# Optimization experiments

Measured on AMD Instinct MI355X. Metric: run time of the kernel, lower is better.

The kernel has to match this reference:

```python
import math
from itertools import permutations
import jax, jax.numpy as jnp
import numpy as np

L, M, D, F, E, N = 64, 3, 3, 32, 8, 100000
PERMS = np.array(list(permutations(range(M))), dtype=np.int32)  # [P, M], P = M! = 6
HALF_PI = math.pi / 2.0
EPS = 1e-8  # torch CosineSimilarity eps


def _atan_inv(s):
    return jnp.arctan(1.0 / s)


def _intra_angle(p):
    # cosine similarity between each row and the previous row (roll by 1 on support axis)
    q = jnp.roll(p, 1, axis=-2)
    num = jnp.sum(q * p, axis=-1)
    den = jnp.maximum(jnp.linalg.norm(q, axis=-1) * jnp.linalg.norm(p, axis=-1), EPS)
    return num / den


def setup_inputs() -> dict:
    key = jax.random.key(0)
    ks = jax.random.split(key, 9)
    return {
        "x_focal": jax.random.normal(ks[0], (N, F), jnp.float32),
        "p_focal": jax.random.normal(ks[1], (N, D), jnp.float32),
        "x_neighbor": jax.random.normal(ks[2], (N, M, F), jnp.float32),
        "p_neighbor": jax.random.normal(ks[3], (N, M, D), jnp.float32),
        "edge_attr_neighbor": jax.random.normal(ks[4], (N, M, E), jnp.float32),
        "x_center": jax.random.normal(ks[5], (L, 1, F), jnp.float32),
        "x_support": jax.random.normal(ks[6], (L, M, F), jnp.float32),
        "edge_attr_support": jax.random.normal(ks[7], (L, M, E), jnp.float32),
        "p_support": jax.random.normal(ks[8], (L, M, D), jnp.float32),
    }


def reference(x_focal, p_focal, x_neighbor, p_neighbor, edge_attr_neighbor,
              x_center, x_support, edge_attr_support, p_support):
    perms = jnp.asarray(PERMS)

    # --- support attribute score over all permutations: sum_{m,f}(x_nei - xs_perm)^2 ---
    xs_p = x_support[:, perms]                                   # [L,P,M,F]
    nei_sq = jnp.sum(x_neighbor * x_neighbor, axis=(1, 2))       # [N]
    sup_sq = jnp.sum(xs_p * xs_p, axis=(2, 3))                   # [L,P]
    cross = jnp.einsum('nmf,lpmf->lpn', x_neighbor, xs_p)        # [L,P,N]
    support_all = _atan_inv(nei_sq[None, None, :] + sup_sq[..., None] - 2.0 * cross)
    best_idx = jnp.argmax(support_all, axis=1)                   # [L,N]
    support_sc = jnp.max(support_all, axis=1)                    # [L,N]

    def select_best(all_sc):  # [L,P,N] -> [L,N] at best permutation
        return jnp.take_along_axis(all_sc, best_idx[:, None, :], axis=1)[:, 0]

    # relative neighbor positions
    p_rel = p_neighbor - p_focal[:, None, :]                     # [N,M,D]
    ps_p = p_support[:, perms]                                   # [L,P,M,D]

    # --- angle score: intra-row cosine angles, then arctan(1/sum_m diff^2) ---
    ang_nei = _intra_angle(p_rel)                                # [N,M]
    ang_sup = _intra_angle(ps_p)                                 # [L,P,M]
    dang = (jnp.sum(ang_nei * ang_nei, axis=-1)[None, None, :]
            + jnp.sum(ang_sup * ang_sup, axis=-1)[..., None]
            - 2.0 * jnp.einsum('nm,lpm->lpn', ang_nei, ang_sup))
    angle_sc = select_best(_atan_inv(dang))                      # [L,N]

    # --- length score: row norms ---
    len_nei = jnp.linalg.norm(p_rel, axis=-1)                    # [N,M]
    len_sup = jnp.linalg.norm(ps_p, axis=-1)                     # [L,P,M]
    dlen = (jnp.sum(len_nei * len_nei, axis=-1)[None, None, :]
            + jnp.sum(len_sup * len_sup, axis=-1)[..., None]
            - 2.0 * jnp.einsum('nm,lpm->lpn', len_nei, len_sup))
    length_sc = select_best(_atan_inv(dlen))                     # [L,N]

    # --- center attribute score ---
    xc = x_center[:, 0, :]                                       # [L,F]
    dc = (jnp.sum(x_focal * x_focal, axis=-1)[None, :]
          + jnp.sum(xc * xc, axis=-1)[:, None]
          - 2.0 * jnp.einsum('nf,lf->ln', x_focal, xc))
    center_sc = _atan_inv(dc)                                    # [L,N]

    # --- edge attribute score ---
    es_p = edge_attr_support[:, perms]                           # [L,P,M,E]
    dedge = (jnp.sum(edge_attr_neighbor ** 2, axis=(1, 2))[None, None, :]
             + jnp.sum(es_p * es_p, axis=(2, 3))[..., None]
             - 2.0 * jnp.einsum('nme,lpme->lpn', edge_attr_neighbor, es_p))
    edge_sc = select_best(_atan_inv(dedge))                      # [L,N]

    # --- total score ---
    h = ((length_sc - HALF_PI) ** 2 + (angle_sc - HALF_PI) ** 2
         + (support_sc - HALF_PI) ** 2 + (center_sc - HALF_PI) ** 2
         + (edge_sc - HALF_PI) ** 2)
    return jnp.arctan(1.0 / h)                                   # [L,N]
```

## Files before the change

### kernel.cpp

```cpp
#include <hip/hip_runtime.h>
#include <math.h>

#define L_ 64
#define HPf 1.57079632679489661923f
#define TIE_THR 4e-3f

typedef _Float16 half4 __attribute__((ext_vector_type(4)));
typedef float    f32x4 __attribute__((ext_vector_type(4)));

#define CVT4(H, L, V) {                                                       \
    _Float16 h0=(_Float16)(V).x, h1=(_Float16)(V).y,                          \
             h2=(_Float16)(V).z, h3=(_Float16)(V).w;                          \
    (H) = (half4){h0, h1, h2, h3};                                            \
    (L) = (half4){(_Float16)((V).x-(float)h0), (_Float16)((V).y-(float)h1),   \
                  (_Float16)((V).z-(float)h2), (_Float16)((V).w-(float)h3)};  \
}

#define MFMA6T(ACC, T, M)                                                           \
    ACC = __builtin_amdgcn_mfma_f32_16x16x16f16(sh[T][0], nh[M][0], ACC, 0, 0, 0); \
    ACC = __builtin_amdgcn_mfma_f32_16x16x16f16(sh[T][0], nl[M][0], ACC, 0, 0, 0); \
    ACC = __builtin_amdgcn_mfma_f32_16x16x16f16(sl[T][0], nh[M][0], ACC, 0, 0, 0); \
    ACC = __builtin_amdgcn_mfma_f32_16x16x16f16(sh[T][1], nh[M][1], ACC, 0, 0, 0); \
    ACC = __builtin_amdgcn_mfma_f32_16x16x16f16(sh[T][1], nl[M][1], ACC, 0, 0, 0); \
    ACC = __builtin_amdgcn_mfma_f32_16x16x16f16(sl[T][1], nh[M][1], ACC, 0, 0, 0);

#define MFMA3(ACC, AH, AL, BH, BL)                                           \
    ACC = __builtin_amdgcn_mfma_f32_16x16x16f16((AH), (BH), ACC, 0, 0, 0);   \
    ACC = __builtin_amdgcn_mfma_f32_16x16x16f16((AH), (BL), ACC, 0, 0, 0);   \
    ACC = __builtin_amdgcn_mfma_f32_16x16x16f16((AL), (BH), ACC, 0, 0, 0);

__global__ __launch_bounds__(64)
void setconvP(const float* __restrict__ x_support,
              const float* __restrict__ edge_sup,
              const float* __restrict__ x_center,
              const float* __restrict__ p_support,
              float* __restrict__ table)
{
    const int l = threadIdx.x;
    if (l >= L_) return;

    const float* xs = x_support + (size_t)l * 96;
    double ssq = 0.0;
    for (int i = 0; i < 96; ++i) { double v = (double)xs[i]; ssq += v * v; }

    const float* es = edge_sup + (size_t)l * 24;
    float esq = 0.f;
    for (int i = 0; i < 24; ++i) esq = fmaf(es[i], es[i], esq);

    const float* xc = x_center + (size_t)l * 32;
    float csq = 0.f;
    for (int i = 0; i < 32; ++i) csq = fmaf(xc[i], xc[i], csq);

    float p0[3], p1[3], p2[3];
    for (int d = 0; d < 3; ++d) {
        p0[d] = p_support[(l * 3 + 0) * 3 + d];
        p1[d] = p_support[(l * 3 + 1) * 3 + d];
        p2[d] = p_support[(l * 3 + 2) * 3 + d];
    }
    float n0 = sqrtf(p0[0]*p0[0] + p0[1]*p0[1] + p0[2]*p0[2]);
    float n1 = sqrtf(p1[0]*p1[0] + p1[1]*p1[1] + p1[2]*p1[2]);
    float n2 = sqrtf(p2[0]*p2[0] + p2[1]*p2[1] + p2[2]*p2[2]);
    float d01 = p0[0]*p1[0] + p0[1]*p1[1] + p0[2]*p1[2];
    float d02 = p0[0]*p2[0] + p0[1]*p2[1] + p0[2]*p2[2];
    float d12 = p1[0]*p2[0] + p1[1]*p2[1] + p1[2]*p2[2];
    float C01 = d01 / fmaxf(n0 * n1, 1e-8f);
    float C02 = d02 / fmaxf(n0 * n2, 1e-8f);
    float C12 = d12 / fmaxf(n1 * n2, 1e-8f);

    float* t = table + l * 16;
    t[0] = n0;  t[1] = n1;  t[2] = n2;
    t[3] = C01; t[4] = C02; t[5] = C12;
    t[6] = C01*C01 + C02*C02 + C12*C12;
    t[7] = n0*n0 + n1*n1 + n2*n2;
    t[8] = esq;
    t[9] = csq;
    t[10] = (float)ssq;
}

__global__ __launch_bounds__(64)
void setconvF(const float* __restrict__ x_neighbor,
              const float* __restrict__ x_support,
              const float* __restrict__ x_focal,
              const float* __restrict__ p_focal,
              const float* __restrict__ p_neighbor,
              const float* __restrict__ edge_nei,
              const float* __restrict__ x_center,
              const float* __restrict__ edge_sup,
              const float* __restrict__ table,
              float* __restrict__ out,
              int* __restrict__ wl_cnt,
              int* __restrict__ wl,
              int wl_cap, int N)
{
    const int lane = threadIdx.x;
    const int j    = lane & 15;
    const int kg   = lane >> 4;
    const int l_w  = blockIdx.y * 16;
    const int n_start = blockIdx.x * 64;

    const float4 z4 = make_float4(0.f, 0.f, 0.f, 0.f);

    half4 sh[4][2], sl[4][2];
    half4 esh[4], esl[4];
    half4 xch[2], xcl[2];
    {
        const int g = j >> 2, e = j & 3;
        #pragma unroll
        for (int t = 0; t < 4; ++t) {
            float4 v0 = z4, v1 = z4, ve = z4;
            if (e < 3) {
                const float* ap = x_support + (size_t)(l_w + 4*t + g) * 96 + e * 32 + kg * 4;
                v0 = *(const float4*)ap;
                v1 = *(const float4*)(ap + 16);
                if (kg < 2)
                    ve = *(const float4*)(edge_sup + (size_t)(l_w + 4*t + g) * 24 + e * 8 + kg * 4);
            }
            CVT4(sh[t][0], sl[t][0], v0);
            CVT4(sh[t][1], sl[t][1], v1);
            CVT4(esh[t], esl[t], ve);
        }
        const int l_c = l_w + 4 * (j & 3) + (j >> 2);
        #pragma unroll
        for (int h = 0; h < 2; ++h) {
            float4 v = *(const float4*)(x_center + (size_t)l_c * 32 + 16*h + kg * 4);
            CVT4(xch[h], xcl[h], v);
        }
    }

    #pragma unroll 1
    for (int c = 0; c < 4; ++c) {
        const int n_j = n_start + c * 16 + j;
        const bool ok = (n_j < N);

        float4 w0h0=z4,w0h1=z4,w1h0=z4,w1h1=z4,w2h0=z4,w2h1=z4;
        float4 ef0=z4, ef1=z4, ef2=z4;
        float4 xf0=z4, xf1=z4;
        float pf0=0.f,pf1=0.f,pf2=0.f;
        float pn0=0.f,pn1=0.f,pn2=0.f,pn3=0.f,pn4=0.f,pn5=0.f,pn6=0.f,pn7=0.f,pn8=0.f;
        if (ok) {
            const float* np = x_neighbor + (size_t)n_j * 96 + kg * 4;
            w0h0 = *(const float4*)(np +  0); w0h1 = *(const float4*)(np + 16);
            w1h0 = *(const float4*)(np + 32); w1h1 = *(const float4*)(np + 48);
            w2h0 = *(const float4*)(np + 64); w2h1 = *(const float4*)(np + 80);
            if (kg < 2) {
                const float* ep = edge_nei + (size_t)n_j * 24 + kg * 4;
                ef0 = *(const float4*)(ep +  0);
                ef1 = *(const float4*)(ep +  8);
                ef2 = *(const float4*)(ep + 16);
            }
            const float* fp = x_focal + (size_t)n_j * 32 + kg * 4;
            xf0 = *(const float4*)(fp + 0);
            xf1 = *(const float4*)(fp + 16);
            pf0 = p_focal[(size_t)n_j*3+0]; pf1 = p_focal[(size_t)n_j*3+1]; pf2 = p_focal[(size_t)n_j*3+2];
            const float* pp = p_neighbor + (size_t)n_j * 9;
            pn0=pp[0]; pn1=pp[1]; pn2=pp[2]; pn3=pp[3]; pn4=pp[4];
            pn5=pp[5]; pn6=pp[6]; pn7=pp[7]; pn8=pp[8];
        }

        float rp = 0.f;
        rp = fmaf(w0h0.x, w0h0.x, rp); rp = fmaf(w0h0.y, w0h0.y, rp);
        rp = fmaf(w0h0.z, w0h0.z, rp); rp = fmaf(w0h0.w, w0h0.w, rp);
        rp = fmaf(w0h1.x, w0h1.x, rp); rp = fmaf(w0h1.y, w0h1.y, rp);
        rp = fmaf(w0h1.z, w0h1.z, rp); rp = fmaf(w0h1.w, w0h1.w, rp);
        rp = fmaf(w1h0.x, w1h0.x, rp); rp = fmaf(w1h0.y, w1h0.y, rp);
        rp = fmaf(w1h0.z, w1h0.z, rp); rp = fmaf(w1h0.w, w1h0.w, rp);
        rp = fmaf(w1h1.x, w1h1.x, rp); rp = fmaf(w1h1.y, w1h1.y, rp);
        rp = fmaf(w1h1.z, w1h1.z, rp); rp = fmaf(w1h1.w, w1h1.w, rp);
        rp = fmaf(w2h0.x, w2h0.x, rp); rp = fmaf(w2h0.y, w2h0.y, rp);
        rp = fmaf(w2h0.z, w2h0.z, rp); rp = fmaf(w2h0.w, w2h0.w, rp);
        rp = fmaf(w2h1.x, w2h1.x, rp); rp = fmaf(w2h1.y, w2h1.y, rp);
        rp = fmaf(w2h1.z, w2h1.z, rp); rp = fmaf(w2h1.w, w2h1.w, rp);
        rp += __shfl_xor(rp, 16);
        rp += __shfl_xor(rp, 32);

        float edsq = 0.f;
        edsq = fmaf(ef0.x, ef0.x, edsq); edsq = fmaf(ef0.y, ef0.y, edsq);
        edsq = fmaf(ef0.z, ef0.z, edsq); edsq = fmaf(ef0.w, ef0.w, edsq);
        edsq = fmaf(ef1.x, ef1.x, edsq); edsq = fmaf(ef1.y, ef1.y, edsq);
        edsq = fmaf(ef1.z, ef1.z, edsq); edsq = fmaf(ef1.w, ef1.w, edsq);
        edsq = fmaf(ef2.x, ef2.x, edsq); edsq = fmaf(ef2.y, ef2.y, edsq);
        edsq = fmaf(ef2.z, ef2.z, edsq); edsq = fmaf(ef2.w, ef2.w, edsq);
        edsq += __shfl_xor(edsq, 16);
        edsq += __shfl_xor(edsq, 32);

        float xfsq = 0.f;
        xfsq = fmaf(xf0.x, xf0.x, xfsq); xfsq = fmaf(xf0.y, xf0.y, xfsq);
        xfsq = fmaf(xf0.z, xf0.z, xfsq); xfsq = fmaf(xf0.w, xf0.w, xfsq);
        xfsq = fmaf(xf1.x, xf1.x, xfsq); xfsq = fmaf(xf1.y, xf1.y, xfsq);
        xfsq = fmaf(xf1.z, xf1.z, xfsq); xfsq = fmaf(xf1.w, xf1.w, xfsq);
        xfsq += __shfl_xor(xfsq, 16);
        xfsq += __shfl_xor(xfsq, 32);

        float pr00=pn0-pf0, pr01=pn1-pf1, pr02=pn2-pf2;
        float pr10=pn3-pf0, pr11=pn4-pf1, pr12=pn5-pf2;
        float pr20=pn6-pf0, pr21=pn7-pf1, pr22=pn8-pf2;
        float lenN0 = sqrtf(pr00*pr00 + pr01*pr01 + pr02*pr02);
        float lenN1 = sqrtf(pr10*pr10 + pr11*pr11 + pr12*pr12);
        float lenN2 = sqrtf(pr20*pr20 + pr21*pr21 + pr22*pr22);
        float angN0 = (pr20*pr00 + pr21*pr01 + pr22*pr02) / fmaxf(lenN2*lenN0, 1e-8f);
        float angN1 = (pr00*pr10 + pr01*pr11 + pr02*pr12) / fmaxf(lenN0*lenN1, 1e-8f);
        float angN2 = (pr10*pr20 + pr11*pr21 + pr12*pr22) / fmaxf(lenN1*lenN2, 1e-8f);
        float angN_sq = angN0*angN0 + angN1*angN1 + angN2*angN2;
        float lenN_sq = lenN0*lenN0 + lenN1*lenN1 + lenN2*lenN2;

        half4 nh[3][2], nl[3][2];
        CVT4(nh[0][0], nl[0][0], w0h0); CVT4(nh[0][1], nl[0][1], w0h1);
        CVT4(nh[1][0], nl[1][0], w1h0); CVT4(nh[1][1], nl[1][1], w1h1);
        CVT4(nh[2][0], nl[2][0], w2h0); CVT4(nh[2][1], nl[2][1], w2h1);
        half4 edh0, edl0, edh1, edl1, edh2, edl2;
        CVT4(edh0, edl0, ef0); CVT4(edh1, edl1, ef1); CVT4(edh2, edl2, ef2);
        half4 xfh0, xfl0, xfh1, xfl1;
        CVT4(xfh0, xfl0, xf0); CVT4(xfh1, xfl1, xf1);

        f32x4 accC = {};
        MFMA3(accC, xch[0], xcl[0], xfh0, xfl0)
        MFMA3(accC, xch[1], xcl[1], xfh1, xfl1)

        #pragma unroll
        for (int t = 0; t < 4; ++t) {
            const int l_t = l_w + 4*t + kg;
            const float* tb = table + l_t * 16;
            f32x4 tb0 = *(const f32x4*)tb;
            f32x4 tb1 = *(const f32x4*)(tb + 4);
            f32x4 tb2 = *(const f32x4*)(tb + 8);

            f32x4 a0 = {}, a1 = {}, a2 = {};
            MFMA6T(a0, t, 0)
            MFMA6T(a1, t, 1)
            MFMA6T(a2, t, 2)

            f32x4 e0 = {}, e1 = {}, e2 = {};
            MFMA3(e0, esh[t], esl[t], edh0, edl0)
            MFMA3(e1, esh[t], esl[t], edh1, edl1)
            MFMA3(e2, esh[t], esl[t], edh2, edl2)

            float c0 = a0[0] + a1[1] + a2[2];
            float c1 = a0[0] + a1[2] + a2[1];
            float c2 = a0[1] + a1[0] + a2[2];
            float c3 = a0[1] + a1[2] + a2[0];
            float c4 = a0[2] + a1[0] + a2[1];
            float c5 = a0[2] + a1[1] + a2[0];

            float b1 = c0, b2 = -3.4e38f; int bpk = 6;
            if (c1 > b1) { b2 = b1; b1 = c1; bpk = 9;  } else if (c1 > b2) b2 = c1;
            if (c2 > b1) { b2 = b1; b1 = c2; bpk = 18; } else if (c2 > b2) b2 = c2;
            if (c3 > b1) { b2 = b1; b1 = c3; bpk = 24; } else if (c3 > b2) b2 = c3;
            if (c4 > b1) { b2 = b1; b1 = c4; bpk = 33; } else if (c4 > b2) b2 = c4;
            if (c5 > b1) { b2 = b1; b1 = c5; bpk = 36; } else if (c5 > b2) b2 = c5;

            const int a = (bpk >> 4) & 3, b = (bpk >> 2) & 3, cc = bpk & 3;

            float se0 = (a  == 0) ? e0[0] : ((a  == 1) ? e0[1] : e0[2]);
            float se1 = (b  == 0) ? e1[0] : ((b  == 1) ? e1[1] : e1[2]);
            float se2 = (cc == 0) ? e2[0] : ((cc == 1) ? e2[1] : e2[2]);
            float bestE = se0 + se1 + se2;

            float la = (a  == 0) ? tb0[0] : ((a  == 1) ? tb0[1] : tb0[2]);
            float lb = (b  == 0) ? tb0[0] : ((b  == 1) ? tb0[1] : tb0[2]);
            float lc = (cc == 0) ? tb0[0] : ((cc == 1) ? tb0[1] : tb0[2]);
            float bestL = fmaf(lenN0, la, fmaf(lenN1, lb, lenN2 * lc));

            float C01 = tb0[3], C02 = tb1[0], C12 = tb1[1];
            int sca = cc + a, sab = a + b, sbc = b + cc;
            float Cca = (sca == 1) ? C01 : ((sca == 2) ? C02 : C12);
            float Cab = (sab == 1) ? C01 : ((sab == 2) ? C02 : C12);
            float Cbc = (sbc == 1) ? C01 : ((sbc == 2) ? C02 : C12);
            float bestA = fmaf(angN0, Cca, fmaf(angN1, Cab, angN2 * Cbc));

            float dist = rp + tb2[2] - 2.0f * b1;
            float t3v = atanf(dist);
            float t1v = atanf(lenN_sq + tb1[3] - 2.0f * bestL);
            float t2v = atanf(angN_sq + tb1[2] - 2.0f * bestA);
            float t4v = atanf(xfsq    + tb2[1] - 2.0f * accC[t]);
            float t5v = atanf(edsq    + tb2[0] - 2.0f * bestE);

            float h = t1v*t1v + t2v*t2v + t3v*t3v + t4v*t4v + t5v*t5v;

            if (ok) {
                size_t idx = (size_t)l_t * N + n_j;
                out[idx] = atanf(1.0f / h);
                if (b1 - b2 <= TIE_THR) {
                    int slot = atomicAdd(wl_cnt, 1);
                    if (slot < wl_cap) wl[slot] = (int)idx;
                }
            }
        }
    }
}

__global__ __launch_bounds__(256)
void setconvA2(const float* __restrict__ x_neighbor,
               const float* __restrict__ x_support,
               const float* __restrict__ x_focal,
               const float* __restrict__ p_focal,
               const float* __restrict__ p_neighbor,
               const float* __restrict__ edge_nei,
               const float* __restrict__ x_center,
               const float* __restrict__ edge_sup,
               const float* __restrict__ table,
               float* __restrict__ out,
               const int* __restrict__ wl_cnt,
               const int* __restrict__ wl,
               int wl_cap, int N)
{
    int cnt = *wl_cnt; if (cnt > wl_cap) cnt = wl_cap;
    const int stride = gridDim.x * blockDim.x;
    for (int i = blockIdx.x * blockDim.x + threadIdx.x; i < cnt; i += stride) {
        const int idx = wl[i];
        const int l = idx / N;
        const int n = idx - l * N;
        const float* xn = x_neighbor + (size_t)n * 96;
        const float* xs = x_support  + (size_t)l * 96;

        double dr[3][3] = {{0,0,0},{0,0,0},{0,0,0}};
        double nei = 0.0;
        for (int f = 0; f < 32; ++f) {
            double a0 = (double)xn[f], a1 = (double)xn[32 + f], a2 = (double)xn[64 + f];
            double b0 = (double)xs[f], b1 = (double)xs[32 + f], b2 = (double)xs[64 + f];
            dr[0][0] += a0 * b0; dr[0][1] += a0 * b1; dr[0][2] += a0 * b2;
            dr[1][0] += a1 * b0; dr[1][1] += a1 * b1; dr[1][2] += a1 * b2;
            dr[2][0] += a2 * b0; dr[2][1] += a2 * b1; dr[2][2] += a2 * b2;
            nei += a0 * a0 + a1 * a1 + a2 * a2;
        }
        double d0 = dr[0][0] + dr[1][1] + dr[2][2];
        double d1 = dr[0][0] + dr[1][2] + dr[2][1];
        double d2 = dr[0][1] + dr[1][0] + dr[2][2];
        double d3 = dr[0][1] + dr[1][2] + dr[2][0];
        double d4 = dr[0][2] + dr[1][0] + dr[2][1];
        double d5 = dr[0][2] + dr[1][1] + dr[2][0];
        double db = d0; int bpk = 6;
        if (d1 > db) { db = d1; bpk = 9;  }
        if (d2 > db) { db = d2; bpk = 18; }
        if (d3 > db) { db = d3; bpk = 24; }
        if (d4 > db) { db = d4; bpk = 33; }
        if (d5 > db) { db = d5; bpk = 36; }
        const int a = (bpk >> 4) & 3, b = (bpk >> 2) & 3, c = bpk & 3;

        const float* tb = table + l * 16;
        float dist = (float)(nei + (double)tb[10] - 2.0 * db);
        float t3v = atanf(dist);

        const float* es = edge_sup + (size_t)l * 24;
        const float* ed = edge_nei + (size_t)n * 24;
        float er[3][3] = {{0,0,0},{0,0,0},{0,0,0}};
        for (int f = 0; f < 8; ++f) {
            float b0 = es[f], b1 = es[8 + f], b2 = es[16 + f];
            float a0 = ed[f], a1 = ed[8 + f], a2 = ed[16 + f];
            er[0][0] = fmaf(a0, b0, er[0][0]);
            er[0][1] = fmaf(a0, b1, er[0][1]);
            er[0][2] = fmaf(a0, b2, er[0][2]);
            er[1][0] = fmaf(a1, b0, er[1][0]);
            er[1][1] = fmaf(a1, b1, er[1][1]);
            er[1][2] = fmaf(a1, b2, er[1][2]);
            er[2][0] = fmaf(a2, b0, er[2][0]);
            er[2][1] = fmaf(a2, b1, er[2][1]);
            er[2][2] = fmaf(a2, b2, er[2][2]);
        }
        float edsq = 0.f;
        for (int f = 0; f < 24; ++f) edsq = fmaf(ed[f], ed[f], edsq);

        const float* xf = x_focal + (size_t)n * 32;
        const float* xc = x_center + (size_t)l * 32;
        float cdot = 0.f, xfsq = 0.f;
        for (int f = 0; f < 32; ++f) {
            cdot = fmaf(xf[f], xc[f], cdot);
            xfsq = fmaf(xf[f], xf[f], xfsq);
        }

        float pf0 = p_focal[(size_t)n*3+0], pf1 = p_focal[(size_t)n*3+1], pf2 = p_focal[(size_t)n*3+2];
        const float* pp = p_neighbor + (size_t)n * 9;
        float pr00=pp[0]-pf0, pr01=pp[1]-pf1, pr02=pp[2]-pf2;
        float pr10=pp[3]-pf0, pr11=pp[4]-pf1, pr12=pp[5]-pf2;
        float pr20=pp[6]-pf0, pr21=pp[7]-pf1, pr22=pp[8]-pf2;
        float lenN0 = sqrtf(pr00*pr00 + pr01*pr01 + pr02*pr02);
        float lenN1 = sqrtf(pr10*pr10 + pr11*pr11 + pr12*pr12);
        float lenN2 = sqrtf(pr20*pr20 + pr21*pr21 + pr22*pr22);
        float angN0 = (pr20*pr00 + pr21*pr01 + pr22*pr02) / fmaxf(lenN2*lenN0, 1e-8f);
        float angN1 = (pr00*pr10 + pr01*pr11 + pr02*pr12) / fmaxf(lenN0*lenN1, 1e-8f);
        float angN2 = (pr10*pr20 + pr11*pr21 + pr12*pr22) / fmaxf(lenN1*lenN2, 1e-8f);
        float angN_sq = angN0*angN0 + angN1*angN1 + angN2*angN2;
        float lenN_sq = lenN0*lenN0 + lenN1*lenN1 + lenN2*lenN2;

        float bestE = er[0][a] + er[1][b] + er[2][c];
        float nv[3] = {tb[0], tb[1], tb[2]};
        float bestL = fmaf(lenN0, nv[a], fmaf(lenN1, nv[b], lenN2 * nv[c]));
        float C01 = tb[3], C02 = tb[4], C12 = tb[5];
        int sca = c + a, sab = a + b, sbc = b + c;
        float Cca = (sca == 1) ? C01 : ((sca == 2) ? C02 : C12);
        float Cab = (sab == 1) ? C01 : ((sab == 2) ? C02 : C12);
        float Cbc = (sbc == 1) ? C01 : ((sbc == 2) ? C02 : C12);
        float bestA = fmaf(angN0, Cca, fmaf(angN1, Cab, angN2 * Cbc));

        float t1v = atanf(lenN_sq + tb[7] - 2.0f * bestL);
        float t2v = atanf(angN_sq + tb[6] - 2.0f * bestA);
        float t4v = atanf(xfsq    + tb[9] - 2.0f * cdot);
        float t5v = atanf(edsq    + tb[8] - 2.0f * bestE);

        float h = t1v*t1v + t2v*t2v + t3v*t3v + t4v*t4v + t5v*t5v;
        out[idx] = atanf(1.0f / h);
    }
}

extern "C" void kernel_launch(void* const* d_in, const int* in_sizes, int n_in,
                              void* d_out, int out_size, void* d_ws, size_t ws_size,
                              hipStream_t stream)
{
    const float* x_focal    = (const float*)d_in[0];
    const float* p_focal    = (const float*)d_in[1];
    const float* x_neighbor = (const float*)d_in[2];
    const float* p_neighbor = (const float*)d_in[3];
    const float* edge_nei   = (const float*)d_in[4];
    const float* x_center   = (const float*)d_in[5];
    const float* x_support  = (const float*)d_in[6];
    const float* edge_sup   = (const float*)d_in[7];
    const float* p_support  = (const float*)d_in[8];
    float* out = (float*)d_out;

    const int N = in_sizes[0] / 32;

    float* table = (float*)d_ws;
    int* wl_cnt = (int*)((char*)d_ws + 4096);
    int* wl     = (int*)((char*)d_ws + 4096 + 16);
    long cap_l = ((long)ws_size - 4096 - 16) / 4;
    int wl_cap = cap_l < 0 ? 0 : (cap_l > 4000000 ? 4000000 : (int)cap_l);

    hipMemsetAsync(wl_cnt, 0, sizeof(int), stream);

    setconvP<<<1, 64, 0, stream>>>(x_support, edge_sup, x_center, p_support, table);

    dim3 gridF((N + 63) / 64, 4);
    setconvF<<<gridF, 64, 0, stream>>>(x_neighbor, x_support, x_focal, p_focal,
                                       p_neighbor, edge_nei, x_center, edge_sup,
                                       table, out, wl_cnt, wl, wl_cap, N);
    setconvA2<<<64, 256, 0, stream>>>(x_neighbor, x_support, x_focal, p_focal,
                                      p_neighbor, edge_nei, x_center, edge_sup,
                                      table, out, wl_cnt, wl, wl_cap, N);
}
```

Baseline: 134.8 us.

## Precompute per-neighbor geometry, prefetch next chunk, and use polynomial atan

Adds a small kernel that computes per-neighbor lengths and angle cosines once and stores eight floats per neighbor, instead of recomputing them in each of the four L-block launches of the main kernel. The main kernel now loads the next 16-neighbor chunk ahead of computing the current one, to hide global memory latency. It also replaces atanf calls with a degree-9 polynomial plus hardware reciprocal. Costs are an extra launch, a workspace layout change, and reduced atan accuracy that may interact with the tie-handling threshold.

```diff
diff --git a/kernel.cpp b/kernel.cpp
--- a/kernel.cpp
+++ b/kernel.cpp
@@ -28,6 +28,28 @@
     ACC = __builtin_amdgcn_mfma_f32_16x16x16f16((AH), (BH), ACC, 0, 0, 0);   \
     ACC = __builtin_amdgcn_mfma_f32_16x16x16f16((AH), (BL), ACC, 0, 0, 0);   \
     ACC = __builtin_amdgcn_mfma_f32_16x16x16f16((AL), (BH), ACC, 0, 0, 0);
+
+__device__ __forceinline__ float atan_poly01(float t) {
+    float t2 = t * t;
+    float p = fmaf(t2, 0.0208351f, -0.0851330f);
+    p = fmaf(t2, p, 0.1801410f);
+    p = fmaf(t2, p, -0.3302995f);
+    p = fmaf(t2, p, 0.9998660f);
+    return t * p;
+}
+__device__ __forceinline__ float fast_atan_abs(float x) {
+    float ax = fabsf(x);
+    float r  = __builtin_amdgcn_rcpf(ax);
+    bool inv = ax > 1.0f;
+    float p  = atan_poly01(inv ? r : ax);
+    return inv ? (HPf - p) : p;
+}
+__device__ __forceinline__ float fast_atan_recip(float h) {
+    float r  = __builtin_amdgcn_rcpf(h);
+    bool inv = h > 1.0f;
+    float p  = atan_poly01(inv ? r : h);
+    return inv ? p : (HPf - p);
+}
 
 __global__ __launch_bounds__(64)
 void setconvP(const float* __restrict__ x_support,
@@ -77,16 +99,41 @@
     t[10] = (float)ssq;
 }
 
+__global__ __launch_bounds__(256)
+void setconvPn(const float* __restrict__ p_focal,
+               const float* __restrict__ p_neighbor,
+               float* __restrict__ nscal, int N)
+{
+    const int n = blockIdx.x * 256 + threadIdx.x;
+    if (n >= N) return;
+    float pf0 = p_focal[(size_t)n*3+0], pf1 = p_focal[(size_t)n*3+1], pf2 = p_focal[(size_t)n*3+2];
+    const float* pp = p_neighbor + (size_t)n * 9;
+    float pr00=pp[0]-pf0, pr01=pp[1]-pf1, pr02=pp[2]-pf2;
+    float pr10=pp[3]-pf0, pr11=pp[4]-pf1, pr12=pp[5]-pf2;
+    float pr20=pp[6]-pf0, pr21=pp[7]-pf1, pr22=pp[8]-pf2;
+    float lenN0 = sqrtf(pr00*pr00 + pr01*pr01 + pr02*pr02);
+    float lenN1 = sqrtf(pr10*pr10 + pr11*pr11 + pr12*pr12);
+    float lenN2 = sqrtf(pr20*pr20 + pr21*pr21 + pr22*pr22);
+    float angN0 = (pr20*pr00 + pr21*pr01 + pr22*pr02) / fmaxf(lenN2*lenN0, 1e-8f);
+    float angN1 = (pr00*pr10 + pr01*pr11 + pr02*pr12) / fmaxf(lenN0*lenN1, 1e-8f);
+    float angN2 = (pr10*pr20 + pr11*pr21 + pr12*pr22) / fmaxf(lenN1*lenN2, 1e-8f);
+    f32x4 a = {lenN0, lenN1, lenN2, angN0};
+    f32x4 b = {angN1, angN2,
+               lenN0*lenN0 + lenN1*lenN1 + lenN2*lenN2,
+               angN0*angN0 + angN1*angN1 + angN2*angN2};
+    *(f32x4*)(nscal + (size_t)n * 8)     = a;
+    *(f32x4*)(nscal + (size_t)n * 8 + 4) = b;
+}
+
 __global__ __launch_bounds__(64)
 void setconvF(const float* __restrict__ x_neighbor,
               const float* __restrict__ x_support,
               const float* __restrict__ x_focal,
-              const float* __restrict__ p_focal,
-              const float* __restrict__ p_neighbor,
               const float* __restrict__ edge_nei,
               const float* __restrict__ x_center,
               const float* __restrict__ edge_sup,
               const float* __restrict__ table,
+              const float* __restrict__ nscal,
               float* __restrict__ out,
               int* __restrict__ wl_cnt,
               int* __restrict__ wl,
@@ -99,6 +146,7 @@
     const int n_start = blockIdx.x * 64;
 
     const float4 z4 = make_float4(0.f, 0.f, 0.f, 0.f);
+    const f32x4  zf = {0.f, 0.f, 0.f, 0.f};
 
     half4 sh[4][2], sl[4][2];
     half4 esh[4], esl[4];
@@ -127,35 +175,42 @@
         }
     }
 
+    float4 Pw0,Pw1,Pw2,Pw3,Pw4,Pw5, Pe0,Pe1,Pe2, Pf0,Pf1;
+    f32x4  Pn0, Pn1;
+
+#define LOADN(CC) {                                                          \
+    const int nn = n_start + (CC) * 16 + j;                                  \
+    const bool okk = (nn < N);                                               \
+    const float* np = x_neighbor + (size_t)nn * 96 + kg * 4;                 \
+    Pw0 = okk ? *(const float4*)(np +  0) : z4;                              \
+    Pw1 = okk ? *(const float4*)(np + 16) : z4;                              \
+    Pw2 = okk ? *(const float4*)(np + 32) : z4;                              \
+    Pw3 = okk ? *(const float4*)(np + 48) : z4;                              \
+    Pw4 = okk ? *(const float4*)(np + 64) : z4;                              \
+    Pw5 = okk ? *(const float4*)(np + 80) : z4;                              \
+    const float* ep = edge_nei + (size_t)nn * 24 + kg * 4;                   \
+    bool oke = okk && (kg < 2);                                              \
+    Pe0 = oke ? *(const float4*)(ep +  0) : z4;                              \
+    Pe1 = oke ? *(const float4*)(ep +  8) : z4;                              \
+    Pe2 = oke ? *(const float4*)(ep + 16) : z4;                              \
+    const float* fp = x_focal + (size_t)nn * 32 + kg * 4;                    \
+    Pf0 = okk ? *(const float4*)(fp +  0) : z4;                              \
+    Pf1 = okk ? *(const float4*)(fp + 16) : z4;                              \
+    Pn0 = okk ? *(const f32x4*)(nscal + (size_t)nn * 8)     : zf;            \
+    Pn1 = okk ? *(const f32x4*)(nscal + (size_t)nn * 8 + 4) : zf;            \
+}
+
+    LOADN(0)
+
     #pragma unroll 1
     for (int c = 0; c < 4; ++c) {
         const int n_j = n_start + c * 16 + j;
         const bool ok = (n_j < N);
 
-        float4 w0h0=z4,w0h1=z4,w1h0=z4,w1h1=z4,w2h0=z4,w2h1=z4;
-        float4 ef0=z4, ef1=z4, ef2=z4;
-        float4 xf0=z4, xf1=z4;
-        float pf0=0.f,pf1=0.f,pf2=0.f;
-        float pn0=0.f,pn1=0.f,pn2=0.f,pn3=0.f,pn4=0.f,pn5=0.f,pn6=0.f,pn7=0.f,pn8=0.f;
-        if (ok) {
-            const float* np = x_neighbor + (size_t)n_j * 96 + kg * 4;
-            w0h0 = *(const float4*)(np +  0); w0h1 = *(const float4*)(np + 16);
-            w1h0 = *(const float4*)(np + 32); w1h1 = *(const float4*)(np + 48);
-            w2h0 = *(const float4*)(np + 64); w2h1 = *(const float4*)(np + 80);
-            if (kg < 2) {
-                const float* ep = edge_nei + (size_t)n_j * 24 + kg * 4;
-                ef0 = *(const float4*)(ep +  0);
-                ef1 = *(const float4*)(ep +  8);
-                ef2 = *(const float4*)(ep + 16);
-            }
-            const float* fp = x_focal + (size_t)n_j * 32 + kg * 4;
-            xf0 = *(const float4*)(fp + 0);
-            xf1 = *(const float4*)(fp + 16);
-            pf0 = p_focal[(size_t)n_j*3+0]; pf1 = p_focal[(size_t)n_j*3+1]; pf2 = p_focal[(size_t)n_j*3+2];
-            const float* pp = p_neighbor + (size_t)n_j * 9;
-            pn0=pp[0]; pn1=pp[1]; pn2=pp[2]; pn3=pp[3]; pn4=pp[4];
-            pn5=pp[5]; pn6=pp[6]; pn7=pp[7]; pn8=pp[8];
-        }
+        float4 w0h0=Pw0, w0h1=Pw1, w1h0=Pw2, w1h1=Pw3, w2h0=Pw4, w2h1=Pw5;
+        float4 ef0=Pe0, ef1=Pe1, ef2=Pe2, xf0=Pf0, xf1=Pf1;
+        f32x4 ns0=Pn0, ns1=Pn1;
+        if (c < 3) LOADN(c + 1)
 
         float rp = 0.f;
         rp = fmaf(w0h0.x, w0h0.x, rp); rp = fmaf(w0h0.y, w0h0.y, rp);
@@ -191,17 +246,9 @@
         xfsq += __shfl_xor(xfsq, 16);
         xfsq += __shfl_xor(xfsq, 32);
 
-        float pr00=pn0-pf0, pr01=pn1-pf1, pr02=pn2-pf2;
-        float pr10=pn3-pf0, pr11=pn4-pf1, pr12=pn5-pf2;
-        float pr20=pn6-pf0, pr21=pn7-pf1, pr22=pn8-pf2;
-        float lenN0 = sqrtf(pr00*pr00 + pr01*pr01 + pr02*pr02);
-        float lenN1 = sqrtf(pr10*pr10 + pr11*pr11 + pr12*pr12);
-        float lenN2 = sqrtf(pr20*pr20 + pr21*pr21 + pr22*pr22);
-        float angN0 = (pr20*pr00 + pr21*pr01 + pr22*pr02) / fmaxf(lenN2*lenN0, 1e-8f);
-        float angN1 = (pr00*pr10 + pr01*pr11 + pr02*pr12) / fmaxf(lenN0*lenN1, 1e-8f);
-        float angN2 = (pr10*pr20 + pr11*pr21 + pr12*pr22) / fmaxf(lenN1*lenN2, 1e-8f);
-        float angN_sq = angN0*angN0 + angN1*angN1 + angN2*angN2;
-        float lenN_sq = lenN0*lenN0 + lenN1*lenN1 + lenN2*lenN2;
+        const float lenN0 = ns0[0], lenN1 = ns0[1], lenN2 = ns0[2];
+        const float angN0 = ns0[3], angN1 = ns1[0], angN2 = ns1[1];
+        const float lenN_sq = ns1[2], angN_sq = ns1[3];
 
         half4 nh[3][2], nl[3][2];
         CVT4(nh[0][0], nl[0][0], w0h0); CVT4(nh[0][1], nl[0][1], w0h1);
@@ -268,17 +315,17 @@
             float bestA = fmaf(angN0, Cca, fmaf(angN1, Cab, angN2 * Cbc));
 
             float dist = rp + tb2[2] - 2.0f * b1;
-            float t3v = atanf(dist);
-            float t1v = atanf(lenN_sq + tb1[3] - 2.0f * bestL);
-            float t2v = atanf(angN_sq + tb1[2] - 2.0f * bestA);
-            float t4v = atanf(xfsq    + tb2[1] - 2.0f * accC[t]);
-            float t5v = atanf(edsq    + tb2[0] - 2.0f * bestE);
+            float t3v = fast_atan_abs(dist);
+            float t1v = fast_atan_abs(lenN_sq + tb1[3] - 2.0f * bestL);
+            float t2v = fast_atan_abs(angN_sq + tb1[2] - 2.0f * bestA);
+            float t4v = fast_atan_abs(xfsq    + tb2[1] - 2.0f * accC[t]);
+            float t5v = fast_atan_abs(edsq    + tb2[0] - 2.0f * bestE);
 
             float h = t1v*t1v + t2v*t2v + t3v*t3v + t4v*t4v + t5v*t5v;
 
             if (ok) {
                 size_t idx = (size_t)l_t * N + n_j;
-                out[idx] = atanf(1.0f / h);
+                out[idx] = fast_atan_recip(h);
                 if (b1 - b2 <= TIE_THR) {
                     int slot = atomicAdd(wl_cnt, 1);
                     if (slot < wl_cap) wl[slot] = (int)idx;
@@ -286,6 +333,7 @@
             }
         }
     }
+#undef LOADN
 }
 
 __global__ __launch_bounds__(256)
@@ -419,19 +467,23 @@
     const int N = in_sizes[0] / 32;
 
     float* table = (float*)d_ws;
-    int* wl_cnt = (int*)((char*)d_ws + 4096);
-    int* wl     = (int*)((char*)d_ws + 4096 + 16);
-    long cap_l = ((long)ws_size - 4096 - 16) / 4;
+    float* nscal = (float*)((char*)d_ws + 4096);
+    size_t cnt_off = 4096 + (size_t)N * 32;
+    cnt_off = (cnt_off + 15) & ~(size_t)15;
+    int* wl_cnt = (int*)((char*)d_ws + cnt_off);
+    int* wl     = (int*)((char*)d_ws + cnt_off + 16);
+    long cap_l = ((long)ws_size - (long)cnt_off - 16) / 4;
     int wl_cap = cap_l < 0 ? 0 : (cap_l > 4000000 ? 4000000 : (int)cap_l);
 
     hipMemsetAsync(wl_cnt, 0, sizeof(int), stream);
 
     setconvP<<<1, 64, 0, stream>>>(x_support, edge_sup, x_center, p_support, table);
+    setconvPn<<<(N + 255) / 256, 256, 0, stream>>>(p_focal, p_neighbor, nscal, N);
 
     dim3 gridF((N + 63) / 64, 4);
-    setconvF<<<gridF, 64, 0, stream>>>(x_neighbor, x_support, x_focal, p_focal,
-                                       p_neighbor, edge_nei, x_center, edge_sup,
-                                       table, out, wl_cnt, wl, wl_cap, N);
+    setconvF<<<gridF, 64, 0, stream>>>(x_neighbor, x_support, x_focal,
+                                       edge_nei, x_center, edge_sup,
+                                       table, nscal, out, wl_cnt, wl, wl_cap, N);
     setconvA2<<<64, 256, 0, stream>>>(x_neighbor, x_support, x_focal, p_focal,
                                       p_neighbor, edge_nei, x_center, edge_sup,
                                       table, out, wl_cnt, wl, wl_cap, N);
```

Result: slower. 198.9 us (+47.6%).
